# Performance work log

Hardware: AMD Instinct MI355X
Metric: run time of the kernel (lower is better)

The kernel has to match this reference:

```python
import jax, jax.numpy as jnp
import numpy as np

DIM = 8192
BATCH = 8

def setup_inputs() -> dict:
    key = jax.random.key(0)
    k1, k2 = jax.random.split(key)
    sdr = jax.random.normal(k1, (BATCH, DIM), dtype=jnp.float32)
    # scale synapse so sigmoid inputs stay in a reasonable range (weights clamped to [-1,1] in torch)
    synapse = jax.random.normal(k2, (DIM, DIM), dtype=jnp.float32) * (1.0 / np.sqrt(DIM))
    return {"sdr": sdr, "synapse": synapse, "steps": 2, "top_k": 60}

def reference(sdr, synapse, steps, top_k):
    # activation propagation: GEMV/GEMM -> sigmoid -> top-k sparsification per step
    act = sdr.astype(jnp.float32)
    B, N = act.shape
    rows = jnp.arange(B)[:, None]  # [B,1] row indices for scatter
    k = min(int(top_k), N)
    for _ in range(int(steps)):
        act = jax.nn.sigmoid(act @ synapse.T)          # [B,N]
        vals, idx = jax.lax.top_k(act, k)              # [B,k]
        act = jnp.zeros_like(act).at[rows, idx].set(vals)  # keep only top-k activations
    return act
```

## Files before the change

kernel.cpp:

```cpp
#include <hip/hip_runtime.h>
#include <cstdint>


#define DIM 8192
#define BATCH 8

__device__ __forceinline__ float sigmoidf_(float x) {
    return 1.0f / (1.0f + __expf(-x));
}

__global__ __launch_bounds__(256) void gemv8_sigmoid(
    const float* __restrict__ A,
    const float* __restrict__ W,
    float* __restrict__ Y)
{
    const int lane = threadIdx.x & 63;
    const int wid  = threadIdx.x >> 6;
    const int gw   = blockIdx.x * 4 + wid;
    const int row0 = gw * 4;
    const int jl   = lane * 4;

    float acc[4][8];
#pragma unroll
    for (int r = 0; r < 4; ++r)
#pragma unroll
        for (int b = 0; b < 8; ++b) acc[r][b] = 0.0f;

    for (int j0 = 0; j0 < DIM; j0 += 256) {
        float4 a[8];
#pragma unroll
        for (int b = 0; b < 8; ++b)
            a[b] = *(const float4*)(A + b * DIM + j0 + jl);
#pragma unroll
        for (int r = 0; r < 4; ++r) {
            const float4 s = *(const float4*)(W + (size_t)(row0 + r) * DIM + j0 + jl);
#pragma unroll
            for (int b = 0; b < 8; ++b) {
                acc[r][b] += s.x * a[b].x;
                acc[r][b] += s.y * a[b].y;
                acc[r][b] += s.z * a[b].z;
                acc[r][b] += s.w * a[b].w;
            }
        }
    }

#pragma unroll
    for (int r = 0; r < 4; ++r) {
#pragma unroll
        for (int b = 0; b < 8; ++b) {
            float v = acc[r][b];
#pragma unroll
            for (int off = 32; off > 0; off >>= 1)
                v += __shfl_down(v, off, 64);
            if (lane == 0)
                Y[b * DIM + row0 + r] = sigmoidf_(v);
        }
    }
}

__global__ __launch_bounds__(256) void topk_sparsify(
    const float* __restrict__ Yin,
    float* __restrict__ Yout,
    const int* __restrict__ kptr)
{
    const int row  = blockIdx.x;
    const int tid  = threadIdx.x;
    const int lane = tid & 63;
    const int wid  = tid >> 6;
    int k = kptr ? *kptr : 60;
    if (k > DIM) k = DIM;

    uint32_t v[32];
    const float* src = Yin + (size_t)row * DIM;
#pragma unroll
    for (int i = 0; i < 32; ++i)
        v[i] = __float_as_uint(src[tid + i * 256]);

    __shared__ int s_part[4];
    __shared__ int s_total;
    __shared__ int s_ctr;

    uint32_t lo = 0u, hi = 0x7F800000u;
    while (hi - lo > 1u) {
        const uint32_t mid = lo + ((hi - lo) >> 1);
        int c = 0;
#pragma unroll
        for (int i = 0; i < 32; ++i) c += (v[i] >= mid) ? 1 : 0;
#pragma unroll
        for (int off = 32; off > 0; off >>= 1)
            c += __shfl_down(c, off, 64);
        if (lane == 0) s_part[wid] = c;
        __syncthreads();
        if (tid == 0) s_total = s_part[0] + s_part[1] + s_part[2] + s_part[3];
        __syncthreads();
        const int tot = s_total;
        __syncthreads();
        if (tot >= k) lo = mid; else hi = mid;
    }
    const uint32_t cutoff = lo;

    {
        int c = 0;
#pragma unroll
        for (int i = 0; i < 32; ++i) c += (v[i] > cutoff) ? 1 : 0;
#pragma unroll
        for (int off = 32; off > 0; off >>= 1)
            c += __shfl_down(c, off, 64);
        if (lane == 0) s_part[wid] = c;
        __syncthreads();
        if (tid == 0) {
            s_total = s_part[0] + s_part[1] + s_part[2] + s_part[3];
            s_ctr = 0;
        }
        __syncthreads();
    }
    const int need_eq = k - s_total;

    float* dst = Yout + (size_t)row * DIM;
#pragma unroll
    for (int i = 0; i < 32; ++i) {
        const uint32_t b = v[i];
        float val = 0.0f;
        if (b > cutoff) {
            val = __uint_as_float(b);
        } else if (b == cutoff) {
            const int pos = atomicAdd(&s_ctr, 1);
            if (pos < need_eq) val = __uint_as_float(b);
        }
        dst[tid + i * 256] = val;
    }
}

extern "C" void kernel_launch(void* const* d_in, const int* in_sizes, int n_in,
                              void* d_out, int out_size, void* d_ws, size_t ws_size,
                              hipStream_t stream) {
    const float* sdr = (const float*)d_in[0];
    const float* syn = (const float*)d_in[1];
    const int* kptr  = (n_in > 3) ? (const int*)d_in[3] : nullptr;
    float* out = (float*)d_out;
    float* tmp = (float*)d_ws;

    gemv8_sigmoid<<<512, 256, 0, stream>>>(sdr, syn, out);
    topk_sparsify<<<8, 256, 0, stream>>>(out, out, kptr);
    gemv8_sigmoid<<<512, 256, 0, stream>>>(out, syn, tmp);
    topk_sparsify<<<8, 256, 0, stream>>>(tmp, out, kptr);
}
```

Baseline: 476.4 us.

## Split GEMV reduction across warps and tighten top-k binary search

The GEMV now gives each block 4 rows and splits the K dimension across its 4 warps, then combines the partial sums through shared memory. This raises the grid from 512 to 2048 blocks to expose more parallelism and memory-level concurrency on the 256 MB weight stream, and it hoists the weight loads ahead of the FMAs. The top-k kernel narrows the search upper bound to 1.0, which is valid because sigmoid outputs lie in [0,1], and it drops one barrier per iteration by having every thread sum the shared partial counts. The costs are one extra shared-memory reduction and barrier per GEMV block.

```diff
diff --git a/kernel.cpp b/kernel.cpp
--- a/kernel.cpp
+++ b/kernel.cpp
@@ -16,8 +16,9 @@
 {
     const int lane = threadIdx.x & 63;
     const int wid  = threadIdx.x >> 6;
-    const int gw   = blockIdx.x * 4 + wid;
-    const int row0 = gw * 4;
+    const int row0 = blockIdx.x * 4;
+    const int jbeg = wid * (DIM / 4);
+    const int jend = jbeg + (DIM / 4);
     const int jl   = lane * 4;
 
     float acc[4][8];
@@ -26,24 +27,28 @@
 #pragma unroll
         for (int b = 0; b < 8; ++b) acc[r][b] = 0.0f;
 
-    for (int j0 = 0; j0 < DIM; j0 += 256) {
+    for (int j0 = jbeg; j0 < jend; j0 += 256) {
         float4 a[8];
 #pragma unroll
         for (int b = 0; b < 8; ++b)
             a[b] = *(const float4*)(A + b * DIM + j0 + jl);
+        float4 wv[4];
+#pragma unroll
+        for (int r = 0; r < 4; ++r)
+            wv[r] = *(const float4*)(W + (size_t)(row0 + r) * DIM + j0 + jl);
 #pragma unroll
         for (int r = 0; r < 4; ++r) {
-            const float4 s = *(const float4*)(W + (size_t)(row0 + r) * DIM + j0 + jl);
 #pragma unroll
             for (int b = 0; b < 8; ++b) {
-                acc[r][b] += s.x * a[b].x;
-                acc[r][b] += s.y * a[b].y;
-                acc[r][b] += s.z * a[b].z;
-                acc[r][b] += s.w * a[b].w;
+                acc[r][b] += wv[r].x * a[b].x;
+                acc[r][b] += wv[r].y * a[b].y;
+                acc[r][b] += wv[r].z * a[b].z;
+                acc[r][b] += wv[r].w * a[b].w;
             }
         }
     }
 
+    __shared__ float part[4][4][8];
 #pragma unroll
     for (int r = 0; r < 4; ++r) {
 #pragma unroll
@@ -52,9 +57,17 @@
 #pragma unroll
             for (int off = 32; off > 0; off >>= 1)
                 v += __shfl_down(v, off, 64);
-            if (lane == 0)
-                Y[b * DIM + row0 + r] = sigmoidf_(v);
+            if (lane == 0) part[wid][r][b] = v;
         }
+    }
+    __syncthreads();
+
+    if (threadIdx.x < 32) {
+        const int r = threadIdx.x >> 3;
+        const int b = threadIdx.x & 7;
+        const float s = part[0][r][b] + part[1][r][b]
+                      + part[2][r][b] + part[3][r][b];
+        Y[b * DIM + row0 + r] = sigmoidf_(s);
     }
 }
 
@@ -77,10 +90,9 @@
         v[i] = __float_as_uint(src[tid + i * 256]);
 
     __shared__ int s_part[4];
-    __shared__ int s_total;
     __shared__ int s_ctr;
 
-    uint32_t lo = 0u, hi = 0x7F800000u;
+    uint32_t lo = 0u, hi = 0x3F800000u;
     while (hi - lo > 1u) {
         const uint32_t mid = lo + ((hi - lo) >> 1);
         int c = 0;
@@ -91,14 +103,13 @@
             c += __shfl_down(c, off, 64);
         if (lane == 0) s_part[wid] = c;
         __syncthreads();
-        if (tid == 0) s_total = s_part[0] + s_part[1] + s_part[2] + s_part[3];
-        __syncthreads();
-        const int tot = s_total;
+        const int tot = s_part[0] + s_part[1] + s_part[2] + s_part[3];
         __syncthreads();
         if (tot >= k) lo = mid; else hi = mid;
     }
     const uint32_t cutoff = lo;
 
+    int needg = 0;
     {
         int c = 0;
 #pragma unroll
@@ -107,14 +118,11 @@
         for (int off = 32; off > 0; off >>= 1)
             c += __shfl_down(c, off, 64);
         if (lane == 0) s_part[wid] = c;
+        if (tid == 0) s_ctr = 0;
         __syncthreads();
-        if (tid == 0) {
-            s_total = s_part[0] + s_part[1] + s_part[2] + s_part[3];
-            s_ctr = 0;
-        }
-        __syncthreads();
+        needg = s_part[0] + s_part[1] + s_part[2] + s_part[3];
     }
-    const int need_eq = k - s_total;
+    const int need_eq = k - needg;
 
     float* dst = Yout + (size_t)row * DIM;
 #pragma unroll
@@ -140,8 +148,8 @@
     float* out = (float*)d_out;
     float* tmp = (float*)d_ws;
 
-    gemv8_sigmoid<<<512, 256, 0, stream>>>(sdr, syn, out);
+    gemv8_sigmoid<<<2048, 256, 0, stream>>>(sdr, syn, out);
     topk_sparsify<<<8, 256, 0, stream>>>(out, out, kptr);
-    gemv8_sigmoid<<<512, 256, 0, stream>>>(out, syn, tmp);
+    gemv8_sigmoid<<<2048, 256, 0, stream>>>(out, syn, tmp);
     topk_sparsify<<<8, 256, 0, stream>>>(tmp, out, kptr);
 }
```

Result: faster. 458.7 us (-3.7%).
